# Kernel tuning notes

Hardware: AMD Instinct MI355X
Metric: run time of the kernel (lower is better)

## Reference

```python
import jax, jax.numpy as jnp
import numpy as np

B, S, E = 2, 2048, 2048
H, DH = 16, 128          # n_head, head_dim
ROT = 32                 # rotary_dim (partial RoPE)
MP = 8                   # mp_num in original forward
MASKED_BIAS = -1e9


def setup_inputs() -> dict:
    key = jax.random.key(0)
    k1, k2, k3 = jax.random.split(key, 3)
    hidden_states = jax.random.normal(k1, (B, S, E), dtype=jnp.float32)
    W_qkv = jax.random.normal(k2, (3 * E, E), dtype=jnp.float32) * (E ** -0.5)
    W_out = jax.random.normal(k3, (E, E), dtype=jnp.float32) * (E ** -0.5)
    return {"hidden_states": hidden_states, "W_qkv": W_qkv, "W_out": W_out}


def _rope_sincos(seq_len, rot_dim, dtype):
    inv_freq = 1.0 / (10000.0 ** (jnp.arange(0, rot_dim, 2, dtype=jnp.float32) / rot_dim))
    ang = jnp.arange(seq_len, dtype=jnp.float32)[:, None] * inv_freq[None, :]  # [S, R/2]
    return jnp.sin(ang).astype(dtype), jnp.cos(ang).astype(dtype)


def _apply_rope(x, sin, cos):
    # x: [B,S,H,R]; sin/cos: [S,R/2] -> repeat_interleave(2) -> [S,R]
    sin2 = jnp.repeat(sin, 2, axis=-1)[None, :, None, :]
    cos2 = jnp.repeat(cos, 2, axis=-1)[None, :, None, :]
    x1 = x[..., ::2]
    x2 = x[..., 1::2]
    rot = jnp.stack((-x2, x1), axis=-1).reshape(x.shape)  # rotate_every_two
    return x * cos2 + rot * sin2


def reference(hidden_states, W_qkv, W_out):
    b, s, e = hidden_states.shape
    # qkv_proj (no bias): torch Linear does x @ W^T
    qkv = jnp.einsum('bse,fe->bsf', hidden_states, W_qkv)          # [B,S,3E]
    qkv = qkv.reshape(b, s, MP, 3 * e // MP)
    q, k, v = jnp.split(qkv, 3, axis=-1)                            # each [B,S,MP,E/MP]
    # _split_heads: flatten mp dim, re-split into heads
    q = q.reshape(b, s, H, DH)
    k = k.reshape(b, s, H, DH)
    v = v.reshape(b, s, H, DH)
    # partial rotary on first ROT dims (q,k in [B,S,H,DH] layout)
    sin, cos = _rope_sincos(s, ROT, hidden_states.dtype)
    q = jnp.concatenate([_apply_rope(q[..., :ROT], sin, cos), q[..., ROT:]], axis=-1)
    k = jnp.concatenate([_apply_rope(k[..., :ROT], sin, cos), k[..., ROT:]], axis=-1)
    # attention: scores / sqrt(DH), causal masked_fill(-1e9), softmax, AV
    scale = jnp.sqrt(jnp.asarray(DH, dtype=jnp.float32)).astype(hidden_states.dtype)
    scores = jnp.einsum('bqhd,bkhd->bhqk', q, k) / scale            # [B,H,S,S]
    causal = jnp.tril(jnp.ones((s, s), dtype=bool))
    scores = jnp.where(causal[None, None], scores, jnp.asarray(MASKED_BIAS, scores.dtype))
    attn = jax.nn.softmax(scores, axis=-1)
    out = jnp.einsum('bhqk,bkhd->bqhd', attn, v)                    # [B,S,H,DH]
    out = out.reshape(b, s, e)
    return jnp.einsum('bse,fe->bsf', out, W_out)                    # out_proj
```

## Files before the change

### kernel.cpp

```cpp
#include <hip/hip_runtime.h>
#include <hip/hip_bf16.h>
#include <cstdint>
#include <cstddef>

using bf16 = __hip_bfloat16;
using short4v = __attribute__((ext_vector_type(4))) short;
using short8 = __attribute__((ext_vector_type(8))) short;
using floatx4 = __attribute__((ext_vector_type(4))) float;

#define MFMA_BF16(A, B, C) __builtin_amdgcn_mfma_f32_16x16x32_bf16((A), (B), (C), 0, 0, 0)

__device__ inline short bf16_bits(float x) {
  bf16 v = __float2bfloat16(x);
  short r;
  __builtin_memcpy(&r, &v, 2);
  return r;
}

__device__ inline void store_c(bf16* p, float v) { *p = __float2bfloat16(v); }
__device__ inline void store_c(float* p, float v) { *p = v; }

__global__ __launch_bounds__(256) void f32_to_bf16_kernel(
    const float* __restrict__ src, bf16* __restrict__ dst, int n8) {
  const int i = blockIdx.x * 256 + threadIdx.x;
  if (i >= n8) return;
  const float4 a = ((const float4*)src)[2 * i];
  const float4 b = ((const float4*)src)[2 * i + 1];
  short8 r;
  r[0] = bf16_bits(a.x); r[1] = bf16_bits(a.y); r[2] = bf16_bits(a.z); r[3] = bf16_bits(a.w);
  r[4] = bf16_bits(b.x); r[5] = bf16_bits(b.y); r[6] = bf16_bits(b.z); r[7] = bf16_bits(b.w);
  *(short8*)(dst + (size_t)i * 8) = r;
}

template <typename TC>
__global__ __launch_bounds__(256) void gemm_bt_async(
    const bf16* __restrict__ A, const bf16* __restrict__ B, TC* __restrict__ C,
    int ldc, int K, bf16* __restrict__ vT, int mpbase) {
  __shared__ bf16 As[128 * 64];
  __shared__ bf16 Bs[128 * 64];
  const int tid = threadIdx.x;
  const int lane = tid & 63;
  const int wave = tid >> 6;
  const int lrow = lane & 15;
  const int quad = lane >> 4;
  const int wm = (wave >> 1) * 64;
  const int wn = (wave & 1) * 64;
  const int tm = blockIdx.y * 128;
  const int tn = blockIdx.x * 128;

  const int srow = tid >> 3;
  const int scl = tid & 7;

  floatx4 acc[4][4] = {};

  for (int k0 = 0; k0 < K; k0 += 64) {
    __syncthreads();
#pragma unroll
    for (int r = 0; r < 4; ++r) {
      const int row = r * 32 + srow;
      const int scg = scl ^ (row & 7);
      __builtin_amdgcn_global_load_lds(
          (const __attribute__((address_space(1))) void*)(A + (size_t)(tm + row) * K + k0 + scg * 8),
          (__attribute__((address_space(3))) void*)(As + row * 64 + scl * 8), 16, 0, 0);
    }
#pragma unroll
    for (int r = 0; r < 4; ++r) {
      const int row = r * 32 + srow;
      const int scg = scl ^ (row & 7);
      __builtin_amdgcn_global_load_lds(
          (const __attribute__((address_space(1))) void*)(B + (size_t)(tn + row) * K + k0 + scg * 8),
          (__attribute__((address_space(3))) void*)(Bs + row * 64 + scl * 8), 16, 0, 0);
    }
    __syncthreads();

#pragma unroll
    for (int kk = 0; kk < 2; ++kk) {
      short8 af[4], bfr[4];
#pragma unroll
      for (int i = 0; i < 4; ++i) {
        const int ra = wm + i * 16 + lrow;
        const int rb = wn + i * 16 + lrow;
        af[i] = *(const short8*)&As[ra * 64 + (((kk * 4 + quad) ^ (ra & 7)) * 8)];
        bfr[i] = *(const short8*)&Bs[rb * 64 + (((kk * 4 + quad) ^ (rb & 7)) * 8)];
      }
#pragma unroll
      for (int i = 0; i < 4; ++i)
#pragma unroll
        for (int j = 0; j < 4; ++j)
          acc[i][j] = MFMA_BF16(af[i], bfr[j], acc[i][j]);
    }
  }

  if (vT != nullptr && ((int)blockIdx.x % 6) >= 4) {
    const int mpl = (int)blockIdx.x / 6;
#pragma unroll
    for (int i = 0; i < 4; ++i)
#pragma unroll
      for (int j = 0; j < 4; ++j) {
        const int fl = tn + wn + j * 16 + lrow;
        const int sv = fl - mpl * 768 - 512;
        const int hh = mpbase + mpl * 2 + (sv >> 7);
        const int dd = sv & 127;
        const int m0 = tm + wm + i * 16 + quad * 4;
        const int bb = m0 >> 11;
        const int ss = m0 & 2047;
        short4v pv;
        pv[0] = bf16_bits(acc[i][j][0]); pv[1] = bf16_bits(acc[i][j][1]);
        pv[2] = bf16_bits(acc[i][j][2]); pv[3] = bf16_bits(acc[i][j][3]);
        *(short4v*)&vT[((size_t)(bb * 16 + hh) * 128 + dd) * 2048 + ss] = pv;
      }
  } else {
#pragma unroll
    for (int i = 0; i < 4; ++i)
#pragma unroll
      for (int j = 0; j < 4; ++j)
#pragma unroll
        for (int r = 0; r < 4; ++r) {
          const int row = tm + wm + i * 16 + quad * 4 + r;
          const int col = tn + wn + j * 16 + lrow;
          store_c(&C[(size_t)row * ldc + col], acc[i][j][r]);
        }
  }
}

__global__ __launch_bounds__(256) void gemm_abf16_bf32(
    const bf16* __restrict__ A, const float* __restrict__ B, float* __restrict__ C,
    int ldc, int K) {
  __shared__ bf16 As[128 * 64];
  __shared__ bf16 Bs[128 * 64];
  const int tid = threadIdx.x;
  const int lane = tid & 63;
  const int wave = tid >> 6;
  const int lrow = lane & 15;
  const int quad = lane >> 4;
  const int wm = (wave >> 1) * 64;
  const int wn = (wave & 1) * 64;
  const int tm = blockIdx.y * 128;
  const int tn = blockIdx.x * 128;

  const int srow = tid >> 3;
  const int scl = tid & 7;
  const int c16 = tid & 15;
  const int br0 = tid >> 4;

  floatx4 acc[4][4] = {};
  float4 breg[8];
#pragma unroll
  for (int r = 0; r < 8; ++r)
    breg[r] = *(const float4*)(B + (size_t)(tn + r * 16 + br0) * K + c16 * 4);

  for (int k0 = 0; k0 < K; k0 += 64) {
    __syncthreads();
#pragma unroll
    for (int r = 0; r < 4; ++r) {
      const int row = r * 32 + srow;
      const int scg = scl ^ (row & 7);
      __builtin_amdgcn_global_load_lds(
          (const __attribute__((address_space(1))) void*)(A + (size_t)(tm + row) * K + k0 + scg * 8),
          (__attribute__((address_space(3))) void*)(As + row * 64 + scl * 8), 16, 0, 0);
    }
#pragma unroll
    for (int r = 0; r < 8; ++r) {
      const int row = r * 16 + br0;
      short4v sv;
      sv[0] = bf16_bits(breg[r].x); sv[1] = bf16_bits(breg[r].y);
      sv[2] = bf16_bits(breg[r].z); sv[3] = bf16_bits(breg[r].w);
      *(short4v*)&Bs[row * 64 + (((c16 >> 1) ^ (row & 7)) * 8) + (c16 & 1) * 4] = sv;
    }
    __syncthreads();
    if (k0 + 64 < K) {
#pragma unroll
      for (int r = 0; r < 8; ++r)
        breg[r] = *(const float4*)(B + (size_t)(tn + r * 16 + br0) * K + k0 + 64 + c16 * 4);
    }

#pragma unroll
    for (int kk = 0; kk < 2; ++kk) {
      short8 af[4], bfr[4];
#pragma unroll
      for (int i = 0; i < 4; ++i) {
        const int ra = wm + i * 16 + lrow;
        const int rb = wn + i * 16 + lrow;
        af[i] = *(const short8*)&As[ra * 64 + (((kk * 4 + quad) ^ (ra & 7)) * 8)];
        bfr[i] = *(const short8*)&Bs[rb * 64 + (((kk * 4 + quad) ^ (rb & 7)) * 8)];
      }
#pragma unroll
      for (int i = 0; i < 4; ++i)
#pragma unroll
        for (int j = 0; j < 4; ++j)
          acc[i][j] = MFMA_BF16(af[i], bfr[j], acc[i][j]);
    }
  }

#pragma unroll
  for (int i = 0; i < 4; ++i)
#pragma unroll
    for (int j = 0; j < 4; ++j)
#pragma unroll
      for (int r = 0; r < 4; ++r) {
        const int row = tm + wm + i * 16 + quad * 4 + r;
        const int col = tn + wn + j * 16 + lrow;
        C[(size_t)row * ldc + col] = acc[i][j][r];
      }
}

__global__ void rope_kernel(bf16* __restrict__ qkv) {
  const int idx = blockIdx.x * 256 + threadIdx.x;
  const int i = idx & 15;
  int t = idx >> 4;
  const int qk = t & 1;
  t >>= 1;
  const int h = t & 15;
  t >>= 4;
  const int s = t & 2047;
  bf16* p = qkv + (size_t)t * 6144 + (h >> 1) * 768 + (h & 1) * 128 + qk * 256 + 2 * i;
  const float x0 = __bfloat162float(p[0]);
  const float x1 = __bfloat162float(p[1]);
  const float inv = powf(10000.f, -(float)(2 * i) / 32.f);
  const float ang = (float)s * inv;
  float sn, cs;
  sincosf(ang, &sn, &cs);
  p[0] = __float2bfloat16(x0 * cs - x1 * sn);
  p[1] = __float2bfloat16(x1 * cs + x0 * sn);
}

__global__ __launch_bounds__(256) void attn_flash_pair(
    const bf16* __restrict__ qkv, const bf16* __restrict__ vT,
    bf16* __restrict__ out) {
  __shared__ short Ks[16 * 128 * 8];
  __shared__ short Vs[16 * 128 * 8];
  __shared__ short Ps[16 * 128 * 8];
  const int tid = threadIdx.x;
  const int wave = tid >> 6;
  const int lane = tid & 63;
  const int lq = lane & 15;
  const int quad = lane >> 4;
  const int h = blockIdx.y;
  const int b = blockIdx.z;
  const size_t SROW = 6144;
  const bf16* base = qkv + (size_t)b * 2048 * SROW;
  const bf16* vbase = vT + (size_t)(b * 16 + h) * 262144;
  const int qoff = (h >> 1) * 768 + (h & 1) * 128;
  const int koff = qoff + 256;
  const float scale = 0.088388347648318447f;

  for (int phase = 0; phase < 2; ++phase) {
    const int qb = phase ? (15 - (int)blockIdx.x) : (int)blockIdx.x;

    short8 qf[2][4];
#pragma unroll
    for (int rt = 0; rt < 2; ++rt) {
      const bf16* qp =
          base + (size_t)(qb * 128 + wave * 32 + rt * 16 + lq) * SROW + qoff + quad * 8;
#pragma unroll
      for (int ks = 0; ks < 4; ++ks) qf[rt][ks] = *(const short8*)(qp + ks * 32);
    }

    floatx4 o[2][8] = {};
    float m_i[2] = {-1e30f, -1e30f};
    float l_acc[2] = {0.f, 0.f};

    const int kb_end = qb + 1;
    for (int kb = 0; kb < kb_end; ++kb) {
      __syncthreads();

#pragma unroll
      for (int i = 0; i < 8; ++i) {
        const int u = wave * 8 + i;
        const int g = u >> 1;
        const int half = (u & 1) * 64;
        __builtin_amdgcn_global_load_lds(
            (const __attribute__((address_space(1))) void*)(
                base + (size_t)(kb * 128 + half + lane) * SROW + koff + g * 8),
            (__attribute__((address_space(3))) void*)(Ks + (g * 128 + half + lane) * 8),
            16, 0, 0);
        __builtin_amdgcn_global_load_lds(
            (const __attribute__((address_space(1))) void*)(
                vbase + (size_t)(half + lane) * 2048 + kb * 128 + g * 8),
            (__attribute__((address_space(3))) void*)(Vs + (g * 128 + half + lane) * 8),
            16, 0, 0);
      }
      __syncthreads();

      floatx4 sc[2][8] = {};
      __builtin_amdgcn_s_setprio(1);
#pragma unroll
      for (int ks = 0; ks < 4; ++ks) {
        const int dg = ks * 4 + quad;
        short8 kf[8];
#pragma unroll
        for (int ct = 0; ct < 8; ++ct)
          kf[ct] = *(const short8*)&Ks[(dg * 128 + ct * 16 + lq) * 8];
#pragma unroll
        for (int rt = 0; rt < 2; ++rt)
#pragma unroll
          for (int ct = 0; ct < 8; ++ct)
            sc[rt][ct] = MFMA_BF16(kf[ct], qf[rt][ks], sc[rt][ct]);
      }
      __builtin_amdgcn_s_setprio(0);

      const int qrow0 = qb * 128 + wave * 32;
      const bool diag = (kb == qb);
#pragma unroll
      for (int rt = 0; rt < 2; ++rt) {
        const int qg = qrow0 + rt * 16 + lq;
        if (diag) {
#pragma unroll
          for (int ct = 0; ct < 8; ++ct)
#pragma unroll
            for (int r = 0; r < 4; ++r)
              if (kb * 128 + ct * 16 + quad * 4 + r > qg) sc[rt][ct][r] = -1e9f;
        }
        float cm[8];
#pragma unroll
        for (int ct = 0; ct < 8; ++ct)
          cm[ct] = fmaxf(fmaxf(sc[rt][ct][0], sc[rt][ct][1]),
                         fmaxf(sc[rt][ct][2], sc[rt][ct][3]));
        float mx = fmaxf(fmaxf(fmaxf(cm[0], cm[1]), fmaxf(cm[2], cm[3])),
                         fmaxf(fmaxf(cm[4], cm[5]), fmaxf(cm[6], cm[7])));
        mx = fmaxf(mx, __shfl_xor(mx, 16, 64));
        mx = fmaxf(mx, __shfl_xor(mx, 32, 64));
        float mcur = m_i[rt];
        if (!__all(mx <= mcur)) {
          const float mnew = fmaxf(mcur, mx);
          const float alpha = __expf((mcur - mnew) * scale);
          m_i[rt] = mnew;
          mcur = mnew;
          l_acc[rt] *= alpha;
#pragma unroll
          for (int dt = 0; dt < 8; ++dt) o[rt][dt] *= alpha;
        }
        float s0 = 0.f, s1 = 0.f, s2 = 0.f, s3 = 0.f;
#pragma unroll
        for (int ct = 0; ct < 8; ++ct) {
          const float p0 = __expf((sc[rt][ct][0] - mcur) * scale);
          const float p1 = __expf((sc[rt][ct][1] - mcur) * scale);
          const float p2 = __expf((sc[rt][ct][2] - mcur) * scale);
          const float p3 = __expf((sc[rt][ct][3] - mcur) * scale);
          sc[rt][ct][0] = p0; sc[rt][ct][1] = p1; sc[rt][ct][2] = p2; sc[rt][ct][3] = p3;
          s0 += p0; s1 += p1; s2 += p2; s3 += p3;
        }
        l_acc[rt] += (s0 + s1) + (s2 + s3);
        const int prow = wave * 32 + rt * 16 + lq;
#pragma unroll
        for (int ct = 0; ct < 8; ++ct) {
          short4v pv;
          pv[0] = bf16_bits(sc[rt][ct][0]); pv[1] = bf16_bits(sc[rt][ct][1]);
          pv[2] = bf16_bits(sc[rt][ct][2]); pv[3] = bf16_bits(sc[rt][ct][3]);
          const int kgrp = ct * 2 + (quad >> 1);
          *(short4v*)&Ps[(kgrp * 128 + prow) * 8 + (quad & 1) * 4] = pv;
        }
      }

      __builtin_amdgcn_s_setprio(1);
#pragma unroll
      for (int kk = 0; kk < 4; ++kk) {
        short8 pf[2], vf[8];
#pragma unroll
        for (int rt = 0; rt < 2; ++rt)
          pf[rt] = *(const short8*)&Ps[((kk * 4 + quad) * 128 + wave * 32 + rt * 16 + lq) * 8];
#pragma unroll
        for (int dt = 0; dt < 8; ++dt)
          vf[dt] = *(const short8*)&Vs[((kk * 4 + quad) * 128 + dt * 16 + lq) * 8];
#pragma unroll
        for (int rt = 0; rt < 2; ++rt)
#pragma unroll
          for (int dt = 0; dt < 8; ++dt)
            o[rt][dt] = MFMA_BF16(vf[dt], pf[rt], o[rt][dt]);
      }
      __builtin_amdgcn_s_setprio(0);
    }

#pragma unroll
    for (int rt = 0; rt < 2; ++rt) {
      float l = l_acc[rt];
      l += __shfl_xor(l, 16, 64);
      l += __shfl_xor(l, 32, 64);
      const float inv_l = 1.f / l;
      const int qg = qb * 128 + wave * 32 + rt * 16 + lq;
      bf16* op = out + ((size_t)(b * 2048 + qg)) * 2048 + h * 128 + quad * 4;
#pragma unroll
      for (int dt = 0; dt < 8; ++dt) {
        short4v s4;
        s4[0] = bf16_bits(o[rt][dt][0] * inv_l);
        s4[1] = bf16_bits(o[rt][dt][1] * inv_l);
        s4[2] = bf16_bits(o[rt][dt][2] * inv_l);
        s4[3] = bf16_bits(o[rt][dt][3] * inv_l);
        *(short4v*)(op + dt * 16) = s4;
      }
    }
  }
}

extern "C" void kernel_launch(void* const* d_in, const int* in_sizes, int n_in,
                              void* d_out, int out_size, void* d_ws, size_t ws_size,
                              hipStream_t stream) {
  const float* hidden = (const float*)d_in[0];
  const float* Wqkv = (const float*)d_in[1];
  const float* Wout = (const float*)d_in[2];
  float* outp = (float*)d_out;

  bf16* qkv = (bf16*)d_ws;
  bf16* flex = qkv + (size_t)4096 * 6144;
  bf16* hbf = (bf16*)d_out;
  bf16* vT = (bf16*)d_out + (size_t)8 * 1024 * 1024;

  f32_to_bf16_kernel<<<4096, 256, 0, stream>>>(hidden, hbf, 1048576);

  f32_to_bf16_kernel<<<3072, 256, 0, stream>>>(Wqkv, flex, 786432);
  gemm_bt_async<bf16><<<dim3(24, 32), 256, 0, stream>>>(hbf, flex, qkv, 6144, 2048, vT, 0);
  f32_to_bf16_kernel<<<3072, 256, 0, stream>>>(Wqkv + (size_t)3072 * 2048, flex, 786432);
  gemm_bt_async<bf16><<<dim3(24, 32), 256, 0, stream>>>(hbf, flex, qkv + 3072, 6144, 2048, vT, 8);

  rope_kernel<<<8192, 256, 0, stream>>>(qkv);

  bf16* attnout = flex;
  attn_flash_pair<<<dim3(8, 16, 2), 256, 0, stream>>>(qkv, vT, attnout);

  gemm_abf16_bf32<<<dim3(16, 32), 256, 0, stream>>>(attnout, Wout, outp, 2048, 2048);
}
```

Before: 432.8 us.

## Swizzle GEMM block order, precompute RoPE table, reuse async GEMM for out_proj

Remaps GEMM block indices with a stride-8 swizzle so that consecutive workgroups are spread across the tile grid, aiming for better cache locality or XCD distribution. RoPE sin and cos values are now computed once into a small table instead of per element with powf and sincosf. The fp32-B out-projection GEMM is replaced by a separate conversion of W_out to bf16 followed by the async-LDS bf16 GEMM. That adds an extra conversion pass and overwrites the qkv workspace after attention, and the RoPE table is placed in flex, which is later reused for the attention output.

After: 422.0 us. 2.5% less time.

```diff
diff --git a/kernel.cpp b/kernel.cpp
--- a/kernel.cpp
+++ b/kernel.cpp
@@ -45,8 +45,15 @@
   const int quad = lane >> 4;
   const int wm = (wave >> 1) * 64;
   const int wn = (wave & 1) * 64;
-  const int tm = blockIdx.y * 128;
-  const int tn = blockIdx.x * 128;
+
+  const int nbx = gridDim.x;
+  const int lin = blockIdx.y * nbx + blockIdx.x;
+  const int cpx = (nbx * gridDim.y) >> 3;
+  const int swz = (lin & 7) * cpx + (lin >> 3);
+  const int bxs = swz % nbx;
+  const int bys = swz / nbx;
+  const int tm = bys * 128;
+  const int tn = bxs * 128;
 
   const int srow = tid >> 3;
   const int scl = tid & 7;
@@ -91,8 +98,8 @@
     }
   }
 
-  if (vT != nullptr && ((int)blockIdx.x % 6) >= 4) {
-    const int mpl = (int)blockIdx.x / 6;
+  if (vT != nullptr && (bxs % 6) >= 4) {
+    const int mpl = bxs / 6;
 #pragma unroll
     for (int i = 0; i < 4; ++i)
 #pragma unroll
@@ -123,88 +130,18 @@
   }
 }
 
-__global__ __launch_bounds__(256) void gemm_abf16_bf32(
-    const bf16* __restrict__ A, const float* __restrict__ B, float* __restrict__ C,
-    int ldc, int K) {
-  __shared__ bf16 As[128 * 64];
-  __shared__ bf16 Bs[128 * 64];
-  const int tid = threadIdx.x;
-  const int lane = tid & 63;
-  const int wave = tid >> 6;
-  const int lrow = lane & 15;
-  const int quad = lane >> 4;
-  const int wm = (wave >> 1) * 64;
-  const int wn = (wave & 1) * 64;
-  const int tm = blockIdx.y * 128;
-  const int tn = blockIdx.x * 128;
-
-  const int srow = tid >> 3;
-  const int scl = tid & 7;
-  const int c16 = tid & 15;
-  const int br0 = tid >> 4;
-
-  floatx4 acc[4][4] = {};
-  float4 breg[8];
-#pragma unroll
-  for (int r = 0; r < 8; ++r)
-    breg[r] = *(const float4*)(B + (size_t)(tn + r * 16 + br0) * K + c16 * 4);
-
-  for (int k0 = 0; k0 < K; k0 += 64) {
-    __syncthreads();
-#pragma unroll
-    for (int r = 0; r < 4; ++r) {
-      const int row = r * 32 + srow;
-      const int scg = scl ^ (row & 7);
-      __builtin_amdgcn_global_load_lds(
-          (const __attribute__((address_space(1))) void*)(A + (size_t)(tm + row) * K + k0 + scg * 8),
-          (__attribute__((address_space(3))) void*)(As + row * 64 + scl * 8), 16, 0, 0);
-    }
-#pragma unroll
-    for (int r = 0; r < 8; ++r) {
-      const int row = r * 16 + br0;
-      short4v sv;
-      sv[0] = bf16_bits(breg[r].x); sv[1] = bf16_bits(breg[r].y);
-      sv[2] = bf16_bits(breg[r].z); sv[3] = bf16_bits(breg[r].w);
-      *(short4v*)&Bs[row * 64 + (((c16 >> 1) ^ (row & 7)) * 8) + (c16 & 1) * 4] = sv;
-    }
-    __syncthreads();
-    if (k0 + 64 < K) {
-#pragma unroll
-      for (int r = 0; r < 8; ++r)
-        breg[r] = *(const float4*)(B + (size_t)(tn + r * 16 + br0) * K + k0 + 64 + c16 * 4);
-    }
-
-#pragma unroll
-    for (int kk = 0; kk < 2; ++kk) {
-      short8 af[4], bfr[4];
-#pragma unroll
-      for (int i = 0; i < 4; ++i) {
-        const int ra = wm + i * 16 + lrow;
-        const int rb = wn + i * 16 + lrow;
-        af[i] = *(const short8*)&As[ra * 64 + (((kk * 4 + quad) ^ (ra & 7)) * 8)];
-        bfr[i] = *(const short8*)&Bs[rb * 64 + (((kk * 4 + quad) ^ (rb & 7)) * 8)];
-      }
-#pragma unroll
-      for (int i = 0; i < 4; ++i)
-#pragma unroll
-        for (int j = 0; j < 4; ++j)
-          acc[i][j] = MFMA_BF16(af[i], bfr[j], acc[i][j]);
-    }
-  }
-
-#pragma unroll
-  for (int i = 0; i < 4; ++i)
-#pragma unroll
-    for (int j = 0; j < 4; ++j)
-#pragma unroll
-      for (int r = 0; r < 4; ++r) {
-        const int row = tm + wm + i * 16 + quad * 4 + r;
-        const int col = tn + wn + j * 16 + lrow;
-        C[(size_t)row * ldc + col] = acc[i][j][r];
-      }
-}
-
-__global__ void rope_kernel(bf16* __restrict__ qkv) {
+__global__ __launch_bounds__(256) void rope_table_kernel(float2* __restrict__ tab) {
+  const int idx = blockIdx.x * 256 + threadIdx.x;
+  const int i = idx & 15;
+  const int s = idx >> 4;
+  const float inv = powf(10000.f, -(float)(2 * i) / 32.f);
+  const float ang = (float)s * inv;
+  float sn, cs;
+  sincosf(ang, &sn, &cs);
+  tab[idx] = make_float2(sn, cs);
+}
+
+__global__ void rope_kernel(bf16* __restrict__ qkv, const float2* __restrict__ tab) {
   const int idx = blockIdx.x * 256 + threadIdx.x;
   const int i = idx & 15;
   int t = idx >> 4;
@@ -216,12 +153,9 @@
   bf16* p = qkv + (size_t)t * 6144 + (h >> 1) * 768 + (h & 1) * 128 + qk * 256 + 2 * i;
   const float x0 = __bfloat162float(p[0]);
   const float x1 = __bfloat162float(p[1]);
-  const float inv = powf(10000.f, -(float)(2 * i) / 32.f);
-  const float ang = (float)s * inv;
-  float sn, cs;
-  sincosf(ang, &sn, &cs);
-  p[0] = __float2bfloat16(x0 * cs - x1 * sn);
-  p[1] = __float2bfloat16(x1 * cs + x0 * sn);
+  const float2 sc2 = tab[(s << 4) + i];
+  p[0] = __float2bfloat16(x0 * sc2.y - x1 * sc2.x);
+  p[1] = __float2bfloat16(x1 * sc2.y + x0 * sc2.x);
 }
 
 __global__ __launch_bounds__(256) void attn_flash_pair(
@@ -404,6 +338,8 @@
   bf16* flex = qkv + (size_t)4096 * 6144;
   bf16* hbf = (bf16*)d_out;
   bf16* vT = (bf16*)d_out + (size_t)8 * 1024 * 1024;
+  bf16* woutbf = qkv;
+  float2* tab = (float2*)flex;
 
   f32_to_bf16_kernel<<<4096, 256, 0, stream>>>(hidden, hbf, 1048576);
 
@@ -412,10 +348,13 @@
   f32_to_bf16_kernel<<<3072, 256, 0, stream>>>(Wqkv + (size_t)3072 * 2048, flex, 786432);
   gemm_bt_async<bf16><<<dim3(24, 32), 256, 0, stream>>>(hbf, flex, qkv + 3072, 6144, 2048, vT, 8);
 
-  rope_kernel<<<8192, 256, 0, stream>>>(qkv);
+  rope_table_kernel<<<128, 256, 0, stream>>>(tab);
+  rope_kernel<<<8192, 256, 0, stream>>>(qkv, tab);
 
   bf16* attnout = flex;
   attn_flash_pair<<<dim3(8, 16, 2), 256, 0, stream>>>(qkv, vT, attnout);
 
-  gemm_abf16_bf32<<<dim3(16, 32), 256, 0, stream>>>(attnout, Wout, outp, 2048, 2048);
-}
+  f32_to_bf16_kernel<<<2048, 256, 0, stream>>>(Wout, woutbf, 524288);
+  gemm_bt_async<float><<<dim3(16, 32), 256, 0, stream>>>(attnout, woutbf, outp, 2048, 2048,
+                                                         (bf16*)nullptr, 0);
+}
```
